# Optimization experiments

Hardware: AMD Instinct MI355X
Metric: run time of the kernel (lower is better)

## Reference

```python
import jax, jax.numpy as jnp
import numpy as np
from jax.ops import segment_sum

NEG_SLOPE = 0.01  # torch F.leaky_relu default

N_NODES = 100000
N_EDGES = 1600000
IN_FEAT = 67
HIDDEN = 256
N_CLASS = 18
N_GRAPHS = 256


def setup_inputs() -> dict:
    key = jax.random.key(0)
    ks = jax.random.split(key, 12)
    h = jax.random.normal(ks[0], (N_NODES, IN_FEAT), dtype=jnp.float32)
    src = jax.random.randint(ks[1], (N_EDGES,), 0, N_NODES, dtype=jnp.int32)
    dst = jax.random.randint(ks[2], (N_EDGES,), 0, N_NODES, dtype=jnp.int32)
    graph_ids = jnp.sort(jax.random.randint(ks[3], (N_NODES,), 0, N_GRAPHS, dtype=jnp.int32))
    s = 0.05
    W1_self = jax.random.normal(ks[4], (IN_FEAT, HIDDEN), dtype=jnp.float32) * s
    W1_neigh = jax.random.normal(ks[5], (IN_FEAT, HIDDEN), dtype=jnp.float32) * s
    b1 = jnp.zeros((HIDDEN,), dtype=jnp.float32)
    W2_self = jax.random.normal(ks[6], (HIDDEN, HIDDEN), dtype=jnp.float32) * s
    W2_neigh = jax.random.normal(ks[7], (HIDDEN, HIDDEN), dtype=jnp.float32) * s
    b2 = jnp.zeros((HIDDEN,), dtype=jnp.float32)
    Wfc = jax.random.normal(ks[8], (HIDDEN, N_CLASS), dtype=jnp.float32) * s
    bfc = jnp.zeros((N_CLASS,), dtype=jnp.float32)
    return {
        "h": h, "W1_self": W1_self, "W1_neigh": W1_neigh, "b1": b1,
        "W2_self": W2_self, "W2_neigh": W2_neigh, "b2": b2,
        "Wfc": Wfc, "bfc": bfc,
        "src": src, "dst": dst, "graph_ids": graph_ids, "num_graphs": N_GRAPHS,
    }


def _sage_mean(h, Wself, Wneigh, b, src, dst, n_nodes):
    # DGL SAGEConv(mean): h_neigh = mean over incoming neighbors; 0 if no neighbors
    agg = segment_sum(h[src], dst, num_segments=n_nodes)          # [N, D]
    deg = segment_sum(jnp.ones_like(dst, dtype=h.dtype), dst, num_segments=n_nodes)
    h_neigh = agg / jnp.maximum(deg, 1.0)[:, None]
    return h @ Wself + h_neigh @ Wneigh + b


def reference(h, W1_self, W1_neigh, b1, W2_self, W2_neigh, b2, Wfc, bfc,
              src, dst, graph_ids, num_graphs):
    n_nodes = h.shape[0]
    x = jax.nn.leaky_relu(_sage_mean(h, W1_self, W1_neigh, b1, src, dst, n_nodes), NEG_SLOPE)
    x = jax.nn.leaky_relu(_sage_mean(x, W2_self, W2_neigh, b2, src, dst, n_nodes), NEG_SLOPE)
    # dgl.mean_nodes: per-graph mean pooling over nodes
    gsum = segment_sum(x, graph_ids, num_segments=num_graphs)       # [G, D]
    gcnt = segment_sum(jnp.ones((n_nodes,), dtype=x.dtype), graph_ids, num_segments=num_graphs)
    hg = gsum / jnp.maximum(gcnt, 1.0)[:, None]
    return hg @ Wfc + bfc  # [G, n_classifier]
```

## Files before the change

### kernel.cpp

```cpp
#include <hip/hip_runtime.h>

#define WAVE 64
#define OW 256
#define LDA1 96
#define NCHUNK 64
#define PBITS 15
#define PBINS (1 << PBITS)
#define NPART 4

typedef short bf16x8 __attribute__((ext_vector_type(8)));
typedef float f32x4  __attribute__((ext_vector_type(4)));

__device__ __forceinline__ unsigned short f2bf(float f) {
    unsigned int u = __float_as_uint(f);
    u = (u + 0x7FFF + ((u >> 16) & 1)) >> 16;
    return (unsigned short)u;
}
__device__ __forceinline__ float bf2f(unsigned short u) {
    return __uint_as_float(((unsigned int)u) << 16);
}
__device__ __forceinline__ float bflo(unsigned int u) { return __uint_as_float(u << 16); }
__device__ __forceinline__ float bfhi(unsigned int u) { return __uint_as_float(u & 0xFFFF0000u); }
__device__ __forceinline__ unsigned int packbf(float lo, float hi) {
    return (unsigned int)f2bf(lo) | ((unsigned int)f2bf(hi) << 16);
}
__device__ __forceinline__ float lrelu(float x) { return x > 0.0f ? x : 0.01f * x; }


__device__ __forceinline__ void pack_b_body(const float* __restrict__ Ws,
                                            const float* __restrict__ Wn,
                                            unsigned short* __restrict__ Bb,
                                            int KHALF, int KT_HALF, int idx) {
    int e  = idx & 7;
    int l  = (idx >> 3) & 63;
    int nt = (idx >> 9) & 15;
    int kt = idx >> 13;
    int n  = nt * 16 + (l & 15);
    int kh = (kt < KT_HALF ? kt : kt - KT_HALF) * 32 + (l >> 4) * 8 + e;
    const float* W = (kt < KT_HALF) ? Ws : Wn;
    float v = (kh < KHALF) ? W[(size_t)kh * OW + n] : 0.0f;
    Bb[idx] = f2bf(v);
}

__global__ void prep_kernel(const float* __restrict__ h, unsigned int* __restrict__ hb,
                            int N, int K,
                            const float* __restrict__ W1s, const float* __restrict__ W1n,
                            unsigned short* __restrict__ Bb1,
                            const float* __restrict__ W2s, const float* __restrict__ W2n,
                            unsigned short* __restrict__ Bb2) {
    const int tid = blockIdx.x * blockDim.x + threadIdx.x;
    const int nth = gridDim.x * blockDim.x;

    const int tot_h = N * (LDA1 / 2);
    for (int i = tid; i < tot_h; i += nth) {
        int row = i / (LDA1 / 2);
        int c   = (i - row * (LDA1 / 2)) * 2;
        float v0 = (c     < K) ? h[(size_t)row * K + c]     : 0.0f;
        float v1 = (c + 1 < K) ? h[(size_t)row * K + c + 1] : 0.0f;
        hb[i] = packbf(v0, v1);
    }
    for (int i = tid; i < 2 * 3 * 16 * 64 * 8; i += nth)
        pack_b_body(W1s, W1n, Bb1, K, 3, i);
    for (int i = tid; i < 2 * 8 * 16 * 64 * 8; i += nth)
        pack_b_body(W2s, W2n, Bb2, OW, 8, i);
}


__global__ __launch_bounds__(512) void hist_kernel(const int* __restrict__ dst, int E, int N,
                                                   unsigned short* __restrict__ hist,
                                                   unsigned short* __restrict__ rank_local) {
    __shared__ unsigned int lcnt[PBINS / 2];
    const int c    = blockIdx.x / NPART;
    const int p    = blockIdx.x - c * NPART;
    const int base = p << PBITS;
    const int nb   = (N - base < PBINS) ? (N - base) : PBINS;
    if (nb <= 0) return;
    const int che = (E + NCHUNK - 1) / NCHUNK;
    const int beg = c * che;
    const int end = (beg + che < E) ? (beg + che) : E;

    for (int i = threadIdx.x; i < PBINS / 2; i += 512) lcnt[i] = 0;
    __syncthreads();

    auto proc = [&](int d, int e) {
        d -= base;
        if ((unsigned)d < (unsigned)nb) {
            unsigned int sh  = (d & 1) * 16;
            unsigned int old = atomicAdd(&lcnt[d >> 1], 1u << sh);
            rank_local[e] = (unsigned short)((old >> sh) & 0xFFFFu);
        }
    };

    if (((beg | end) & 3) == 0) {
        const int4* dst4 = (const int4*)(dst + beg);
        const int n4 = (end - beg) >> 2;
        for (int i = threadIdx.x; i < n4; i += 512) {
            int4 d = dst4[i];
            int e = beg + 4 * i;
            proc(d.x, e + 0);
            proc(d.y, e + 1);
            proc(d.z, e + 2);
            proc(d.w, e + 3);
        }
    } else {
        for (int e = beg + (int)threadIdx.x; e < end; e += 512)
            proc(dst[e], e);
    }
    __syncthreads();

    unsigned short* hrow = hist + (size_t)c * N + base;
    for (int i = threadIdx.x; i < nb; i += 512) {
        unsigned int v = lcnt[i >> 1];
        hrow[i] = (unsigned short)((v >> ((i & 1) * 16)) & 0xFFFFu);
    }
}

__global__ void chunk_scan_kernel(unsigned short* __restrict__ hist, int* __restrict__ cnt,
                                  int N) {
    int bin = blockIdx.x * blockDim.x + threadIdx.x;
    if (bin >= N) return;
    int s = 0;
#pragma unroll 8
    for (int c = 0; c < NCHUNK; ++c) {
        size_t idx = (size_t)c * N + bin;
        int t = hist[idx];
        hist[idx] = (unsigned short)s;
        s += t;
    }
    cnt[bin] = s;
}

__global__ __launch_bounds__(1024) void scan_blocksum(const int* __restrict__ cnt,
                                                      int* __restrict__ bsum, int n) {
    __shared__ int s[1024];
    int i = blockIdx.x * 1024 + threadIdx.x;
    s[threadIdx.x] = (i < n) ? cnt[i] : 0;
    __syncthreads();
    for (int off = 512; off > 0; off >>= 1) {
        if (threadIdx.x < off) s[threadIdx.x] += s[threadIdx.x + off];
        __syncthreads();
    }
    if (threadIdx.x == 0) bsum[blockIdx.x] = s[0];
}

__global__ __launch_bounds__(128) void scan_offsets(int* __restrict__ bsum, int nb) {
    __shared__ int s[128];
    int v = (threadIdx.x < nb) ? bsum[threadIdx.x] : 0;
    s[threadIdx.x] = v;
    __syncthreads();
    for (int off = 1; off < 128; off <<= 1) {
        int t = (threadIdx.x >= off) ? s[threadIdx.x - off] : 0;
        __syncthreads();
        s[threadIdx.x] += t;
        __syncthreads();
    }
    if (threadIdx.x < nb) bsum[threadIdx.x] = s[threadIdx.x] - v;
}

__global__ __launch_bounds__(1024) void scan_write(const int* __restrict__ cnt,
                                                   const int* __restrict__ boff,
                                                   int* __restrict__ rowptr, int n) {
    __shared__ int s[1024];
    int i = blockIdx.x * 1024 + threadIdx.x;
    int v = (i < n) ? cnt[i] : 0;
    s[threadIdx.x] = v;
    __syncthreads();
    for (int off = 1; off < 1024; off <<= 1) {
        int t = (threadIdx.x >= off) ? s[threadIdx.x - off] : 0;
        __syncthreads();
        s[threadIdx.x] += t;
        __syncthreads();
    }
    if (i < n) rowptr[i + 1] = boff[blockIdx.x] + s[threadIdx.x];
    if (i == 0) rowptr[0] = 0;
}

__global__ void fill_kernel(const int* __restrict__ src, const int* __restrict__ dst,
                            const unsigned short* __restrict__ rank_local,
                            const int* __restrict__ rowptr,
                            const unsigned short* __restrict__ hist,
                            int* __restrict__ csr, int E, int N) {
    const int che = (E + NCHUNK - 1) / NCHUNK;
    const int tid = blockIdx.x * blockDim.x + threadIdx.x;
    const int nth = gridDim.x * blockDim.x;

    if ((che & 3) == 0) {
        const int e4 = E >> 2;
        const int4* dst4 = (const int4*)dst;
        const int4* src4 = (const int4*)src;
        const ushort4* r4 = (const ushort4*)rank_local;
        for (int i = tid; i < e4; i += nth) {
            int4 d = dst4[i];
            int4 s = src4[i];
            ushort4 r = r4[i];
            const unsigned short* hrow = hist + (size_t)(4 * i / che) * N;
            csr[rowptr[d.x] + (int)hrow[d.x] + (int)r.x] = s.x;
            csr[rowptr[d.y] + (int)hrow[d.y] + (int)r.y] = s.y;
            csr[rowptr[d.z] + (int)hrow[d.z] + (int)r.z] = s.z;
            csr[rowptr[d.w] + (int)hrow[d.w] + (int)r.w] = s.w;
        }
        for (int e = e4 * 4 + tid; e < E; e += nth) {
            int d = dst[e];
            csr[rowptr[d] + (int)hist[(size_t)(e / che) * N + d] + (int)rank_local[e]] = src[e];
        }
    } else {
        for (int e = tid; e < E; e += nth) {
            int d = dst[e];
            csr[rowptr[d] + (int)hist[(size_t)(e / che) * N + d] + (int)rank_local[e]] = src[e];
        }
    }
}


__global__ void gather_mean256_half(const unsigned int* __restrict__ feat,
                                    const int* __restrict__ rowptr, const int* __restrict__ csr,
                                    unsigned int* __restrict__ aggm, int N, int colhalf) {
    const int lane = threadIdx.x & (WAVE - 1);
    const int grp  = lane >> 4;
    const int sub  = lane & 15;
    const int cb   = colhalf * 64;
    int wave = (blockIdx.x * blockDim.x + threadIdx.x) / WAVE;
    int nw   = (gridDim.x * blockDim.x) / WAVE;

    for (int v = wave; v < N; v += nw) {
        const int beg = rowptr[v], deg = rowptr[v + 1] - beg;
        float l0 = 0.f, h0 = 0.f, l1 = 0.f, h1 = 0.f,
              l2 = 0.f, h2 = 0.f, l3 = 0.f, h3 = 0.f;

        const int noct = deg >> 3;
        for (int i = 0; i < noct; ++i) {
            int e0 = csr[beg + 8 * i + grp];
            int e1 = csr[beg + 8 * i + 4 + grp];
            uint4 x0 = *(const uint4*)(feat + (size_t)e0 * 128 + cb + sub * 4);
            uint4 x1 = *(const uint4*)(feat + (size_t)e1 * 128 + cb + sub * 4);
            l0 += bflo(x0.x) + bflo(x1.x); h0 += bfhi(x0.x) + bfhi(x1.x);
            l1 += bflo(x0.y) + bflo(x1.y); h1 += bfhi(x0.y) + bfhi(x1.y);
            l2 += bflo(x0.z) + bflo(x1.z); h2 += bfhi(x0.z) + bfhi(x1.z);
            l3 += bflo(x0.w) + bflo(x1.w); h3 += bfhi(x0.w) + bfhi(x1.w);
        }
        for (int e = (noct << 3) + grp; e < deg; e += 4) {
            int s = csr[beg + e];
            uint4 x = *(const uint4*)(feat + (size_t)s * 128 + cb + sub * 4);
            l0 += bflo(x.x); h0 += bfhi(x.x);
            l1 += bflo(x.y); h1 += bfhi(x.y);
            l2 += bflo(x.z); h2 += bfhi(x.z);
            l3 += bflo(x.w); h3 += bfhi(x.w);
        }
        l0 += __shfl_xor(l0, 16); l0 += __shfl_xor(l0, 32);
        h0 += __shfl_xor(h0, 16); h0 += __shfl_xor(h0, 32);
        l1 += __shfl_xor(l1, 16); l1 += __shfl_xor(l1, 32);
        h1 += __shfl_xor(h1, 16); h1 += __shfl_xor(h1, 32);
        l2 += __shfl_xor(l2, 16); l2 += __shfl_xor(l2, 32);
        h2 += __shfl_xor(h2, 16); h2 += __shfl_xor(h2, 32);
        l3 += __shfl_xor(l3, 16); l3 += __shfl_xor(l3, 32);
        h3 += __shfl_xor(h3, 16); h3 += __shfl_xor(h3, 32);

        if (grp == 0) {
            float inv = 1.0f / fmaxf((float)deg, 1.0f);
            uint4 o;
            o.x = packbf(l0 * inv, h0 * inv);
            o.y = packbf(l1 * inv, h1 * inv);
            o.z = packbf(l2 * inv, h2 * inv);
            o.w = packbf(l3 * inv, h3 * inv);
            *(uint4*)(aggm + (size_t)v * 128 + cb + sub * 4) = o;
        }
    }
}

__global__ void gather_mean_pad(const unsigned int* __restrict__ feat,
                                const int* __restrict__ rowptr, const int* __restrict__ csr,
                                unsigned int* __restrict__ aggm, int N) {
    const int lane = threadIdx.x & (WAVE - 1);
    const int half = lane >> 5;
    const int sub  = lane & 31;
    const bool act = sub < 24;
    int wave = (blockIdx.x * blockDim.x + threadIdx.x) / WAVE;
    int nw   = (gridDim.x * blockDim.x) / WAVE;

    for (int v = wave; v < N; v += nw) {
        const int beg = rowptr[v], deg = rowptr[v + 1] - beg;
        const int npairs = deg >> 1;
        float l0 = 0.f, h0 = 0.f, l1 = 0.f, h1 = 0.f;

        int p = 0;
        for (; p + 3 < npairs; p += 4) {
            int i0 = csr[beg + 2 * (p + 0) + half];
            int i1 = csr[beg + 2 * (p + 1) + half];
            int i2 = csr[beg + 2 * (p + 2) + half];
            int i3 = csr[beg + 2 * (p + 3) + half];
            if (act) {
                uint2 x0 = *(const uint2*)(feat + (size_t)i0 * 48 + sub * 2);
                uint2 x1 = *(const uint2*)(feat + (size_t)i1 * 48 + sub * 2);
                uint2 x2 = *(const uint2*)(feat + (size_t)i2 * 48 + sub * 2);
                uint2 x3 = *(const uint2*)(feat + (size_t)i3 * 48 + sub * 2);
                l0 += bflo(x0.x) + bflo(x1.x) + bflo(x2.x) + bflo(x3.x);
                h0 += bfhi(x0.x) + bfhi(x1.x) + bfhi(x2.x) + bfhi(x3.x);
                l1 += bflo(x0.y) + bflo(x1.y) + bflo(x2.y) + bflo(x3.y);
                h1 += bfhi(x0.y) + bfhi(x1.y) + bfhi(x2.y) + bfhi(x3.y);
            }
        }
        for (; p < npairs; ++p) {
            int i0 = csr[beg + 2 * p + half];
            if (act) {
                uint2 x0 = *(const uint2*)(feat + (size_t)i0 * 48 + sub * 2);
                l0 += bflo(x0.x); h0 += bfhi(x0.x);
                l1 += bflo(x0.y); h1 += bfhi(x0.y);
            }
        }
        if ((deg & 1) && half == 0) {
            int i0 = csr[beg + deg - 1];
            if (act) {
                uint2 x0 = *(const uint2*)(feat + (size_t)i0 * 48 + sub * 2);
                l0 += bflo(x0.x); h0 += bfhi(x0.x);
                l1 += bflo(x0.y); h1 += bfhi(x0.y);
            }
        }
        l0 += __shfl_xor(l0, 32); h0 += __shfl_xor(h0, 32);
        l1 += __shfl_xor(l1, 32); h1 += __shfl_xor(h1, 32);

        if (half == 0 && act) {
            float inv = 1.0f / fmaxf((float)deg, 1.0f);
            uint2 o;
            o.x = packbf(l0 * inv, h0 * inv);
            o.y = packbf(l1 * inv, h1 * inv);
            *(uint2*)(aggm + (size_t)v * 48 + sub * 2) = o;
        }
    }
}

template<int KT_HALF, int CHUNK>
__global__ __launch_bounds__(256) void sage_mfma(
    const unsigned short* __restrict__ Hs, const unsigned short* __restrict__ Hn, int lda,
    const unsigned short* __restrict__ Bb, const float* __restrict__ bias,
    unsigned short* __restrict__ outb, int M)
{
    constexpr int NT    = 2 * KT_HALF;
    constexpr int NCH   = NT / CHUNK;
    constexpr int CELEM = CHUNK * 16 * 64;
    constexpr int CPT   = CELEM / 256;
    __shared__ bf16x8 Bs[CELEM];

    const int t    = threadIdx.x;
    const int lane = t & 63, wid = t >> 6;
    const int wm   = wid >> 1, wn = wid & 1;
    const int brow = blockIdx.x * 64;
    const int lrow = lane & 15, kblk = lane >> 4;

    const int r0 = brow + wm * 32 + lrow;
    const int r1 = r0 + 16;
    const int r0c = (r0 < M) ? r0 : (M - 1);
    const int r1c = (r1 < M) ? r1 : (M - 1);

    f32x4 acc[2][8];
#pragma unroll
    for (int rt = 0; rt < 2; ++rt)
#pragma unroll
        for (int ct = 0; ct < 8; ++ct) acc[rt][ct] = (f32x4)0.0f;

    for (int ch = 0; ch < NCH; ++ch) {
        bf16x8 a0[CHUNK], a1[CHUNK];
#pragma unroll
        for (int k = 0; k < CHUNK; ++k) {
            int kt = ch * CHUNK + k;
            bool self = kt < KT_HALF;
            int kh = (self ? kt : kt - KT_HALF) * 32 + kblk * 8;
            const unsigned short* srcp = self ? Hs : Hn;
            a0[k] = *(const bf16x8*)(srcp + (size_t)r0c * lda + kh);
            a1[k] = *(const bf16x8*)(srcp + (size_t)r1c * lda + kh);
        }
        const bf16x8* gB = (const bf16x8*)Bb + (size_t)ch * CELEM;
        bf16x8 tmp[CPT];
#pragma unroll
        for (int i = 0; i < CPT; ++i) tmp[i] = gB[i * 256 + t];
        __syncthreads();
#pragma unroll
        for (int i = 0; i < CPT; ++i) Bs[i * 256 + t] = tmp[i];
        __syncthreads();
#pragma unroll
        for (int k = 0; k < CHUNK; ++k) {
            const bf16x8* bp = &Bs[(k * 16 + wn * 8) * 64 + lane];
#pragma unroll
            for (int ct = 0; ct < 8; ++ct) {
                bf16x8 b = bp[ct * 64];
                acc[0][ct] = __builtin_amdgcn_mfma_f32_16x16x32_bf16(a0[k], b, acc[0][ct], 0, 0, 0);
                acc[1][ct] = __builtin_amdgcn_mfma_f32_16x16x32_bf16(a1[k], b, acc[1][ct], 0, 0, 0);
            }
        }
    }

#pragma unroll
    for (int rt = 0; rt < 2; ++rt) {
        int rbase = brow + wm * 32 + rt * 16 + kblk * 4;
#pragma unroll
        for (int ct = 0; ct < 8; ++ct) {
            int col = wn * 128 + ct * 16 + lrow;
            float vb = bias[col];
#pragma unroll
            for (int j = 0; j < 4; ++j) {
                int row = rbase + j;
                if (row < M)
                    outb[(size_t)row * OW + col] = f2bf(lrelu(acc[rt][ct][j] + vb));
            }
        }
    }
}


__global__ __launch_bounds__(256) void pool_fc_kernel(
    const unsigned short* __restrict__ x, const int* __restrict__ gid,
    const float* __restrict__ Wfc, const float* __restrict__ bfc,
    float* __restrict__ out, int N, int C)
{
    int g = blockIdx.x;
    int lo = 0, hi = N;
    while (lo < hi) { int m = (lo + hi) >> 1; if (gid[m] < g) lo = m + 1; else hi = m; }
    int beg = lo;
    hi = N;
    while (lo < hi) { int m = (lo + hi) >> 1; if (gid[m] <= g) lo = m + 1; else hi = m; }
    int end = lo;

    __shared__ float hg[OW];
    int c = threadIdx.x;
    float s0 = 0.f, s1 = 0.f, s2 = 0.f, s3 = 0.f;
    int r = beg;
    for (; r + 3 < end; r += 4) {
        s0 += bf2f(x[(size_t)(r + 0) * OW + c]);
        s1 += bf2f(x[(size_t)(r + 1) * OW + c]);
        s2 += bf2f(x[(size_t)(r + 2) * OW + c]);
        s3 += bf2f(x[(size_t)(r + 3) * OW + c]);
    }
    for (; r < end; ++r) s0 += bf2f(x[(size_t)r * OW + c]);
    float s = (s0 + s1) + (s2 + s3);
    float inv = (end > beg) ? 1.0f / (float)(end - beg) : 0.0f;
    hg[c] = s * inv;
    __syncthreads();

    if (c < C) {
        float a = bfc[c];
        for (int k = 0; k < OW; ++k)
            a = fmaf(hg[k], Wfc[(size_t)k * C + c], a);
        out[(size_t)g * C + c] = a;
    }
}

extern "C" void kernel_launch(void* const* d_in, const int* in_sizes, int n_in,
                              void* d_out, int out_size, void* d_ws, size_t ws_size,
                              hipStream_t stream) {
    const float* h   = (const float*)d_in[0];
    const float* W1s = (const float*)d_in[1];
    const float* W1n = (const float*)d_in[2];
    const float* b1  = (const float*)d_in[3];
    const float* W2s = (const float*)d_in[4];
    const float* W2n = (const float*)d_in[5];
    const float* b2  = (const float*)d_in[6];
    const float* Wfc = (const float*)d_in[7];
    const float* bfc = (const float*)d_in[8];
    const int*   src = (const int*)d_in[9];
    const int*   dst = (const int*)d_in[10];
    const int*   gid = (const int*)d_in[11];

    const int N  = in_sizes[11];
    const int E  = in_sizes[9];
    const int K1 = in_sizes[0] / N;
    const int NC = in_sizes[8];
    const int G  = out_size / NC;

    char* w = (char*)d_ws;
    auto alloc = [&](size_t bytes) { char* p = w; w += (bytes + 255) & ~(size_t)255; return p; };
    unsigned int*   hb     = (unsigned int*)alloc((size_t)N * (LDA1 / 2) * 4);
    unsigned int*   agg1b  = (unsigned int*)alloc((size_t)N * (LDA1 / 2) * 4);
    unsigned short* x1b    = (unsigned short*)alloc((size_t)N * OW * 2);
    unsigned short* agg2b  = (unsigned short*)alloc((size_t)N * OW * 2);
    int*            rowptr = (int*)alloc((size_t)(N + 1) * 4);
    int*            cnt    = (int*)alloc((size_t)N * 4);
    int*            csr    = (int*)alloc((size_t)E * 4);
    unsigned short* rankl  = (unsigned short*)alloc((size_t)E * 2);
    unsigned short* hist   = (unsigned short*)alloc((size_t)NCHUNK * N * 2);
    int*            bsum   = (int*)alloc(1024 * 4);
    unsigned short* Bb1    = (unsigned short*)alloc((size_t)2 * 3 * 16 * 64 * 8 * 2);
    unsigned short* Bb2    = (unsigned short*)alloc((size_t)2 * 8 * 16 * 64 * 8 * 2);

    float* out = (float*)d_out;
    const int nb = (N + 1023) / 1024;

    hist_kernel<<<NCHUNK * NPART, 512, 0, stream>>>(dst, E, N, hist, rankl);
    chunk_scan_kernel<<<(N + 255) / 256, 256, 0, stream>>>(hist, cnt, N);
    scan_blocksum<<<nb, 1024, 0, stream>>>(cnt, bsum, N);
    scan_offsets<<<1, 128, 0, stream>>>(bsum, nb);
    scan_write<<<nb, 1024, 0, stream>>>(cnt, bsum, rowptr, N);
    fill_kernel<<<2048, 256, 0, stream>>>(src, dst, rankl, rowptr, hist, csr, E, N);

    prep_kernel<<<2048, 256, 0, stream>>>(h, hb, N, K1, W1s, W1n, Bb1, W2s, W2n, Bb2);

    const int gemm_grid = (N + 63) / 64;

    gather_mean_pad<<<4096, 256, 0, stream>>>(hb, rowptr, csr, agg1b, N);
    sage_mfma<3, 2><<<gemm_grid, 256, 0, stream>>>((const unsigned short*)hb,
                                                   (const unsigned short*)agg1b, LDA1,
                                                   Bb1, b1, x1b, N);

    gather_mean256_half<<<4096, 256, 0, stream>>>((const unsigned int*)x1b, rowptr, csr,
                                                  (unsigned int*)agg2b, N, 0);
    gather_mean256_half<<<4096, 256, 0, stream>>>((const unsigned int*)x1b, rowptr, csr,
                                                  (unsigned int*)agg2b, N, 1);
    sage_mfma<8, 2><<<gemm_grid, 256, 0, stream>>>(x1b, agg2b, OW, Bb2, b2, x1b, N);

    pool_fc_kernel<<<G, 256, 0, stream>>>(x1b, gid, Wfc, bfc, out, N, NC);
}
```

Measured before the change: 408.6 us.

## Gather neighbor features from FP8 copies to halve gather traffic

Adds FP8 (e4m3) copies of the input features and of the layer-1 output, written by the prep kernel and the first GEMM epilogue. Both neighbor-mean gathers now read 1-byte features instead of bf16, and the layer-2 gather handles all 256 columns in one pass instead of two half-width passes. This targets the random-access gather bandwidth, which dominates aggregation. The cost is extra writes for the FP8 copies and reduced precision in the aggregated means, which may push accuracy past tolerance.

```diff
diff --git a/kernel.cpp b/kernel.cpp
--- a/kernel.cpp
+++ b/kernel.cpp
@@ -10,6 +10,7 @@
 
 typedef short bf16x8 __attribute__((ext_vector_type(8)));
 typedef float f32x4  __attribute__((ext_vector_type(4)));
+typedef float f32x2  __attribute__((ext_vector_type(2)));
 
 __device__ __forceinline__ unsigned short f2bf(float f) {
     unsigned int u = __float_as_uint(f);
@@ -25,6 +26,20 @@
     return (unsigned int)f2bf(lo) | ((unsigned int)f2bf(hi) << 16);
 }
 __device__ __forceinline__ float lrelu(float x) { return x > 0.0f ? x : 0.01f * x; }
+
+__device__ __forceinline__ unsigned int pack4_f8(float v0, float v1, float v2, float v3) {
+    int p = __builtin_amdgcn_cvt_pk_fp8_f32(v0, v1, 0, false);
+    p = __builtin_amdgcn_cvt_pk_fp8_f32(v2, v3, p, true);
+    return (unsigned int)p;
+}
+__device__ __forceinline__ unsigned char enc1_f8(float v) {
+    return (unsigned char)(__builtin_amdgcn_cvt_pk_fp8_f32(v, 0.0f, 0, false) & 0xFF);
+}
+__device__ __forceinline__ void acc4_f8(float* a, unsigned int u) {
+    f32x2 lo = __builtin_amdgcn_cvt_pk_f32_fp8(u, false);
+    f32x2 hi = __builtin_amdgcn_cvt_pk_f32_fp8(u, true);
+    a[0] += lo.x; a[1] += lo.y; a[2] += hi.x; a[3] += hi.y;
+}
 
 
 __device__ __forceinline__ void pack_b_body(const float* __restrict__ Ws,
@@ -43,7 +58,7 @@
 }
 
 __global__ void prep_kernel(const float* __restrict__ h, unsigned int* __restrict__ hb,
-                            int N, int K,
+                            unsigned int* __restrict__ hb8, int N, int K,
                             const float* __restrict__ W1s, const float* __restrict__ W1n,
                             unsigned short* __restrict__ Bb1,
                             const float* __restrict__ W2s, const float* __restrict__ W2n,
@@ -58,6 +73,17 @@
         float v0 = (c     < K) ? h[(size_t)row * K + c]     : 0.0f;
         float v1 = (c + 1 < K) ? h[(size_t)row * K + c + 1] : 0.0f;
         hb[i] = packbf(v0, v1);
+    }
+    const int tot8 = N * (LDA1 / 4);
+    for (int i = tid; i < tot8; i += nth) {
+        int row = i / (LDA1 / 4);
+        int c   = (i - row * (LDA1 / 4)) * 4;
+        const float* hr = h + (size_t)row * K;
+        float v0 = (c     < K) ? hr[c]     : 0.0f;
+        float v1 = (c + 1 < K) ? hr[c + 1] : 0.0f;
+        float v2 = (c + 2 < K) ? hr[c + 2] : 0.0f;
+        float v3 = (c + 3 < K) ? hr[c + 3] : 0.0f;
+        hb8[i] = pack4_f8(v0, v1, v2, v3);
     }
     for (int i = tid; i < 2 * 3 * 16 * 64 * 8; i += nth)
         pack_b_body(W1s, W1n, Bb1, K, 3, i);
@@ -212,64 +238,59 @@
 }
 
 
-__global__ void gather_mean256_half(const unsigned int* __restrict__ feat,
-                                    const int* __restrict__ rowptr, const int* __restrict__ csr,
-                                    unsigned int* __restrict__ aggm, int N, int colhalf) {
+__global__ void gather_mean256_f8(const unsigned char* __restrict__ feat,
+                                  const int* __restrict__ rowptr, const int* __restrict__ csr,
+                                  unsigned int* __restrict__ aggm, int N) {
     const int lane = threadIdx.x & (WAVE - 1);
     const int grp  = lane >> 4;
     const int sub  = lane & 15;
-    const int cb   = colhalf * 64;
     int wave = (blockIdx.x * blockDim.x + threadIdx.x) / WAVE;
     int nw   = (gridDim.x * blockDim.x) / WAVE;
 
     for (int v = wave; v < N; v += nw) {
         const int beg = rowptr[v], deg = rowptr[v + 1] - beg;
-        float l0 = 0.f, h0 = 0.f, l1 = 0.f, h1 = 0.f,
-              l2 = 0.f, h2 = 0.f, l3 = 0.f, h3 = 0.f;
+        float a[16];
+#pragma unroll
+        for (int i = 0; i < 16; ++i) a[i] = 0.0f;
 
         const int noct = deg >> 3;
         for (int i = 0; i < noct; ++i) {
             int e0 = csr[beg + 8 * i + grp];
             int e1 = csr[beg + 8 * i + 4 + grp];
-            uint4 x0 = *(const uint4*)(feat + (size_t)e0 * 128 + cb + sub * 4);
-            uint4 x1 = *(const uint4*)(feat + (size_t)e1 * 128 + cb + sub * 4);
-            l0 += bflo(x0.x) + bflo(x1.x); h0 += bfhi(x0.x) + bfhi(x1.x);
-            l1 += bflo(x0.y) + bflo(x1.y); h1 += bfhi(x0.y) + bfhi(x1.y);
-            l2 += bflo(x0.z) + bflo(x1.z); h2 += bfhi(x0.z) + bfhi(x1.z);
-            l3 += bflo(x0.w) + bflo(x1.w); h3 += bfhi(x0.w) + bfhi(x1.w);
+            uint4 x0 = *(const uint4*)(feat + (size_t)e0 * 256 + sub * 16);
+            uint4 x1 = *(const uint4*)(feat + (size_t)e1 * 256 + sub * 16);
+            acc4_f8(a + 0,  x0.x); acc4_f8(a + 4,  x0.y);
+            acc4_f8(a + 8,  x0.z); acc4_f8(a + 12, x0.w);
+            acc4_f8(a + 0,  x1.x); acc4_f8(a + 4,  x1.y);
+            acc4_f8(a + 8,  x1.z); acc4_f8(a + 12, x1.w);
         }
         for (int e = (noct << 3) + grp; e < deg; e += 4) {
             int s = csr[beg + e];
-            uint4 x = *(const uint4*)(feat + (size_t)s * 128 + cb + sub * 4);
-            l0 += bflo(x.x); h0 += bfhi(x.x);
-            l1 += bflo(x.y); h1 += bfhi(x.y);
-            l2 += bflo(x.z); h2 += bfhi(x.z);
-            l3 += bflo(x.w); h3 += bfhi(x.w);
-        }
-        l0 += __shfl_xor(l0, 16); l0 += __shfl_xor(l0, 32);
-        h0 += __shfl_xor(h0, 16); h0 += __shfl_xor(h0, 32);
-        l1 += __shfl_xor(l1, 16); l1 += __shfl_xor(l1, 32);
-        h1 += __shfl_xor(h1, 16); h1 += __shfl_xor(h1, 32);
-        l2 += __shfl_xor(l2, 16); l2 += __shfl_xor(l2, 32);
-        h2 += __shfl_xor(h2, 16); h2 += __shfl_xor(h2, 32);
-        l3 += __shfl_xor(l3, 16); l3 += __shfl_xor(l3, 32);
-        h3 += __shfl_xor(h3, 16); h3 += __shfl_xor(h3, 32);
-
+            uint4 x = *(const uint4*)(feat + (size_t)s * 256 + sub * 16);
+            acc4_f8(a + 0,  x.x); acc4_f8(a + 4,  x.y);
+            acc4_f8(a + 8,  x.z); acc4_f8(a + 12, x.w);
+        }
+#pragma unroll
+        for (int i = 0; i < 16; ++i) {
+            a[i] += __shfl_xor(a[i], 16);
+            a[i] += __shfl_xor(a[i], 32);
+        }
         if (grp == 0) {
             float inv = 1.0f / fmaxf((float)deg, 1.0f);
-            uint4 o;
-            o.x = packbf(l0 * inv, h0 * inv);
-            o.y = packbf(l1 * inv, h1 * inv);
-            o.z = packbf(l2 * inv, h2 * inv);
-            o.w = packbf(l3 * inv, h3 * inv);
-            *(uint4*)(aggm + (size_t)v * 128 + cb + sub * 4) = o;
-        }
-    }
-}
-
-__global__ void gather_mean_pad(const unsigned int* __restrict__ feat,
-                                const int* __restrict__ rowptr, const int* __restrict__ csr,
-                                unsigned int* __restrict__ aggm, int N) {
+            unsigned int o[8];
+#pragma unroll
+            for (int i = 0; i < 8; ++i)
+                o[i] = packbf(a[2 * i] * inv, a[2 * i + 1] * inv);
+            unsigned int* dst0 = aggm + (size_t)v * 128 + sub * 8;
+            *(uint4*)(dst0)     = make_uint4(o[0], o[1], o[2], o[3]);
+            *(uint4*)(dst0 + 4) = make_uint4(o[4], o[5], o[6], o[7]);
+        }
+    }
+}
+
+__global__ void gather_mean_pad_f8(const unsigned char* __restrict__ feat,
+                                   const int* __restrict__ rowptr, const int* __restrict__ csr,
+                                   unsigned int* __restrict__ aggm, int N) {
     const int lane = threadIdx.x & (WAVE - 1);
     const int half = lane >> 5;
     const int sub  = lane & 31;
@@ -280,7 +301,7 @@
     for (int v = wave; v < N; v += nw) {
         const int beg = rowptr[v], deg = rowptr[v + 1] - beg;
         const int npairs = deg >> 1;
-        float l0 = 0.f, h0 = 0.f, l1 = 0.f, h1 = 0.f;
+        float a[4] = {0.f, 0.f, 0.f, 0.f};
 
         int p = 0;
         for (; p + 3 < npairs; p += 4) {
@@ -289,50 +310,45 @@
             int i2 = csr[beg + 2 * (p + 2) + half];
             int i3 = csr[beg + 2 * (p + 3) + half];
             if (act) {
-                uint2 x0 = *(const uint2*)(feat + (size_t)i0 * 48 + sub * 2);
-                uint2 x1 = *(const uint2*)(feat + (size_t)i1 * 48 + sub * 2);
-                uint2 x2 = *(const uint2*)(feat + (size_t)i2 * 48 + sub * 2);
-                uint2 x3 = *(const uint2*)(feat + (size_t)i3 * 48 + sub * 2);
-                l0 += bflo(x0.x) + bflo(x1.x) + bflo(x2.x) + bflo(x3.x);
-                h0 += bfhi(x0.x) + bfhi(x1.x) + bfhi(x2.x) + bfhi(x3.x);
-                l1 += bflo(x0.y) + bflo(x1.y) + bflo(x2.y) + bflo(x3.y);
-                h1 += bfhi(x0.y) + bfhi(x1.y) + bfhi(x2.y) + bfhi(x3.y);
+                unsigned int x0 = *(const unsigned int*)(feat + (size_t)i0 * 96 + sub * 4);
+                unsigned int x1 = *(const unsigned int*)(feat + (size_t)i1 * 96 + sub * 4);
+                unsigned int x2 = *(const unsigned int*)(feat + (size_t)i2 * 96 + sub * 4);
+                unsigned int x3 = *(const unsigned int*)(feat + (size_t)i3 * 96 + sub * 4);
+                acc4_f8(a, x0); acc4_f8(a, x1); acc4_f8(a, x2); acc4_f8(a, x3);
             }
         }
         for (; p < npairs; ++p) {
             int i0 = csr[beg + 2 * p + half];
             if (act) {
-                uint2 x0 = *(const uint2*)(feat + (size_t)i0 * 48 + sub * 2);
-                l0 += bflo(x0.x); h0 += bfhi(x0.x);
-                l1 += bflo(x0.y); h1 += bfhi(x0.y);
+                unsigned int x0 = *(const unsigned int*)(feat + (size_t)i0 * 96 + sub * 4);
+                acc4_f8(a, x0);
             }
         }
         if ((deg & 1) && half == 0) {
             int i0 = csr[beg + deg - 1];
             if (act) {
-                uint2 x0 = *(const uint2*)(feat + (size_t)i0 * 48 + sub * 2);
-                l0 += bflo(x0.x); h0 += bfhi(x0.x);
-                l1 += bflo(x0.y); h1 += bfhi(x0.y);
+                unsigned int x0 = *(const unsigned int*)(feat + (size_t)i0 * 96 + sub * 4);
+                acc4_f8(a, x0);
             }
         }
-        l0 += __shfl_xor(l0, 32); h0 += __shfl_xor(h0, 32);
-        l1 += __shfl_xor(l1, 32); h1 += __shfl_xor(h1, 32);
+#pragma unroll
+        for (int i = 0; i < 4; ++i) a[i] += __shfl_xor(a[i], 32);
 
         if (half == 0 && act) {
             float inv = 1.0f / fmaxf((float)deg, 1.0f);
             uint2 o;
-            o.x = packbf(l0 * inv, h0 * inv);
-            o.y = packbf(l1 * inv, h1 * inv);
+            o.x = packbf(a[0] * inv, a[1] * inv);
+            o.y = packbf(a[2] * inv, a[3] * inv);
             *(uint2*)(aggm + (size_t)v * 48 + sub * 2) = o;
         }
     }
 }
 
-template<int KT_HALF, int CHUNK>
+template<int KT_HALF, int CHUNK, bool F8OUT>
 __global__ __launch_bounds__(256) void sage_mfma(
     const unsigned short* __restrict__ Hs, const unsigned short* __restrict__ Hn, int lda,
     const unsigned short* __restrict__ Bb, const float* __restrict__ bias,
-    unsigned short* __restrict__ outb, int M)
+    unsigned short* __restrict__ outb, unsigned char* __restrict__ out8, int M)
 {
     constexpr int NT    = 2 * KT_HALF;
     constexpr int NCH   = NT / CHUNK;
@@ -398,8 +414,12 @@
 #pragma unroll
             for (int j = 0; j < 4; ++j) {
                 int row = rbase + j;
-                if (row < M)
-                    outb[(size_t)row * OW + col] = f2bf(lrelu(acc[rt][ct][j] + vb));
+                if (row < M) {
+                    float v = lrelu(acc[rt][ct][j] + vb);
+                    outb[(size_t)row * OW + col] = f2bf(v);
+                    if (F8OUT)
+                        out8[(size_t)row * OW + col] = enc1_f8(v);
+                }
             }
         }
     }
@@ -468,8 +488,10 @@
     char* w = (char*)d_ws;
     auto alloc = [&](size_t bytes) { char* p = w; w += (bytes + 255) & ~(size_t)255; return p; };
     unsigned int*   hb     = (unsigned int*)alloc((size_t)N * (LDA1 / 2) * 4);
+    unsigned int*   hb8    = (unsigned int*)alloc((size_t)N * LDA1);
     unsigned int*   agg1b  = (unsigned int*)alloc((size_t)N * (LDA1 / 2) * 4);
     unsigned short* x1b    = (unsigned short*)alloc((size_t)N * OW * 2);
+    unsigned char*  x1f8   = (unsigned char*)alloc((size_t)N * OW);
     unsigned short* agg2b  = (unsigned short*)alloc((size_t)N * OW * 2);
     int*            rowptr = (int*)alloc((size_t)(N + 1) * 4);
     int*            cnt    = (int*)alloc((size_t)N * 4);
@@ -490,20 +512,20 @@
     scan_write<<<nb, 1024, 0, stream>>>(cnt, bsum, rowptr, N);
     fill_kernel<<<2048, 256, 0, stream>>>(src, dst, rankl, rowptr, hist, csr, E, N);
 
-    prep_kernel<<<2048, 256, 0, stream>>>(h, hb, N, K1, W1s, W1n, Bb1, W2s, W2n, Bb2);
+    prep_kernel<<<2048, 256, 0, stream>>>(h, hb, hb8, N, K1, W1s, W1n, Bb1, W2s, W2n, Bb2);
 
     const int gemm_grid = (N + 63) / 64;
 
-    gather_mean_pad<<<4096, 256, 0, stream>>>(hb, rowptr, csr, agg1b, N);
-    sage_mfma<3, 2><<<gemm_grid, 256, 0, stream>>>((const unsigned short*)hb,
-                                                   (const unsigned short*)agg1b, LDA1,
-                                                   Bb1, b1, x1b, N);
-
-    gather_mean256_half<<<4096, 256, 0, stream>>>((const unsigned int*)x1b, rowptr, csr,
-                                                  (unsigned int*)agg2b, N, 0);
-    gather_mean256_half<<<4096, 256, 0, stream>>>((const unsigned int*)x1b, rowptr, csr,
-                                                  (unsigned int*)agg2b, N, 1);
-    sage_mfma<8, 2><<<gemm_grid, 256, 0, stream>>>(x1b, agg2b, OW, Bb2, b2, x1b, N);
+    gather_mean_pad_f8<<<4096, 256, 0, stream>>>((const unsigned char*)hb8, rowptr, csr,
+                                                 agg1b, N);
+    sage_mfma<3, 2, true><<<gemm_grid, 256, 0, stream>>>((const unsigned short*)hb,
+                                                         (const unsigned short*)agg1b, LDA1,
+                                                         Bb1, b1, x1b, x1f8, N);
+
+    gather_mean256_f8<<<4096, 256, 0, stream>>>(x1f8, rowptr, csr,
+                                                (unsigned int*)agg2b, N);
+    sage_mfma<8, 2, false><<<gemm_grid, 256, 0, stream>>>(x1b, agg2b, OW, Bb2, b2,
+                                                          x1b, nullptr, N);
 
     pool_fc_kernel<<<G, 256, 0, stream>>>(x1b, gid, Wfc, bfc, out, N, NC);
 }
```

Result: faster. 357.9 us (-12.4%).
